# Optimization experiments

Measured on AMD Instinct MI355X. Metric: run time of the kernel, lower is better.

## Reference

```python
import jax, jax.numpy as jnp
import numpy as np

RADIUS = 0.4
NSHELLS = 3
GSCALE = 0.69314718056 * NSHELLS ** 2  # ln(2)*num_shells^2, as in TFN.__init__
KNN = 32          # patch_size
UNITS = 64        # per-type intertwiner width
STRIDE = 4        # source->target pooling ratio (num_points[i]/num_points[i+1])


def real_sh(d):
    """Real spherical harmonics up to l=3 on unit vectors d[...,3] -> [...,16]."""
    x, y, z = d[..., 0], d[..., 1], d[..., 2]
    x2, y2, z2 = x * x, y * y, z * z
    comps = [
        0.282095 * jnp.ones_like(x),                 # l=0
        0.488603 * y, 0.488603 * z, 0.488603 * x,    # l=1 (y,z,x)
        1.092548 * x * y,                            # l=2
        1.092548 * y * z,
        0.315392 * (3.0 * z2 - 1.0),
        1.092548 * x * z,
        0.546274 * (x2 - y2),
        0.590044 * y * (3.0 * x2 - y2),              # l=3
        2.890611 * x * y * z,
        0.457046 * y * (5.0 * z2 - 1.0),
        0.373176 * z * (5.0 * z2 - 3.0),
        0.457046 * x * (5.0 * z2 - 1.0),
        1.445306 * z * (x2 - y2),
        0.590044 * x * (x2 - 3.0 * y2),
    ]
    return jnp.stack(comps, axis=-1)


def setup_inputs() -> dict:
    key = jax.random.key(0)
    ks = jax.random.split(key, 16)
    B, N, C = 32, 2048, 64
    SC = NSHELLS * C  # channels after shell expansion
    FEAT = 4 * UNITS  # invariant feature dim (types 0..3)
    NUM_CLASSES = 40
    inp = {
        "points": jax.random.normal(ks[0], (B, N, 3), jnp.float32),
        "feats": 0.1 * jax.random.normal(ks[1], (B, N, C), jnp.float32),
        "W0": jax.random.normal(ks[2], (SC, UNITS), jnp.float32) / np.sqrt(SC),
        "b0": jnp.zeros((UNITS,), jnp.float32),
        "W1": jax.random.normal(ks[3], (SC, UNITS), jnp.float32) / np.sqrt(SC),
        "W2": jax.random.normal(ks[4], (SC, UNITS), jnp.float32) / np.sqrt(SC),
        "W3": jax.random.normal(ks[5], (SC, UNITS), jnp.float32) / np.sqrt(SC),
        "Wfc1": jax.random.normal(ks[6], (FEAT, 512), jnp.float32) / np.sqrt(FEAT),
        "bfc1": jnp.zeros((512,), jnp.float32),
        "Wfc2": jax.random.normal(ks[7], (512, 256), jnp.float32) / np.sqrt(512),
        "bfc2": jnp.zeros((256,), jnp.float32),
        "Wsm": jax.random.normal(ks[8], (256, NUM_CLASSES), jnp.float32) / np.sqrt(256),
        "bsm": jnp.zeros((NUM_CLASSES,), jnp.float32),
    }
    return inp


def reference(points, feats, W0, b0, W1, W2, W3, Wfc1, bfc1, Wfc2, bfc2, Wsm, bsm):
    # --- pooling: strided subsample (kd_pooling analogue) ---
    target = points[:, ::STRIDE]                       # [B,M,3]
    # --- ball-query style grouping: knn gather ---
    d2 = jnp.sum((target[:, :, None, :] - points[:, None, :, :]) ** 2, axis=-1)  # [B,M,N]
    _, idx = jax.lax.top_k(-d2, KNN)                   # [B,M,K]
    gat = jax.vmap(lambda a, i: a[i])
    p = gat(points, idx)                               # [B,M,K,3]
    f = gat(feats, idx)                                # [B,M,K,C]
    rel = p - target[:, :, None, :]
    dist = jnp.sqrt(jnp.maximum(jnp.sum(rel * rel, axis=-1), 1e-12))  # [B,M,K]
    dirs = rel / dist[..., None]
    # --- spherical-harmonic Gaussian shell kernels ---
    Y = real_sh(dirs)                                  # [B,M,K,16]
    centers = jnp.linspace(0.0, 1.0, NSHELLS)
    dn = dist / RADIUS
    w = jnp.exp(-GSCALE * (dn[..., None] - centers) ** 2)
    w = w * (dn <= 1.0)[..., None]                     # bounded kernel
    w = w / (jnp.sum(w, axis=2, keepdims=True) + 1e-8)  # normalize over patch
    kern = w[..., :, None] * Y[..., None, :]           # [B,M,K,S,16]
    # --- point conv: contract over patch dim ---
    z = jnp.einsum('bmksp,bmkc->bmpsc', kern, f)       # [B,M,16,S,C]
    B_, M_ = z.shape[:2]
    z = z.reshape(B_, M_, 16, -1)                      # [B,M,16,S*C]
    # --- per-type Dense intertwiners (bias only on type-0) + invariant norms ---
    slabs = [(0, 1, W0, b0), (1, 4, W1, None), (4, 9, W2, None), (9, 16, W3, None)]
    outs = []
    for s, e, W, b in slabs:
        o = z[:, :, s:e, :] @ W
        if b is not None:
            o = o + b
        outs.append(jnp.sqrt(jnp.maximum(jnp.sum(o * o, axis=2), 1e-8)))  # [B,M,U]
    h = jnp.concatenate(outs, axis=-1)                 # [B,M,4U]
    h = jnp.max(h, axis=1)                             # global max pool
    # --- MLP head ---
    h = jax.nn.relu(h @ Wfc1 + bfc1)
    h = jax.nn.relu(h @ Wfc2 + bfc2)
    return jax.nn.softmax(h @ Wsm + bsm, axis=-1)
```

## Files before the change

### kernel.cpp

```cpp
#include <hip/hip_runtime.h>
#include <hip/hip_bf16.h>
#include <math.h>

#define B_ 32
#define N_ 2048
#define C_ 64
#define M_ 512
#define KNN_ 32
#define RADIUS_ 0.4f
#define RCUT2 0.16016f
#define GSCALE_ 6.2383246250f
#define TT 4
#define NWAVE 8
#define SEGCAP 40
#define NBLK 4096

typedef __attribute__((ext_vector_type(8))) short bf16x8;
typedef __attribute__((ext_vector_type(4))) float f32x4;
union FragU { uint4 q; bf16x8 h; unsigned int u[4]; };

#define ZT_ 3208
#define ZTH (ZT_*2)
#define RSTH 200
#define ZLOFF 3200
#define FSH 560
#define CAND_OFF 6416
#define WGT_OFF  12832
#define WGT_TS   96
#define SM_TOTAL 13216

__device__ inline unsigned cvt_pk_bf16(float a, float b) {
    unsigned r;
    asm("v_cvt_pk_bf16_f32 %0, %1, %2" : "=v"(r) : "v"(a), "v"(b));
    return r;
}

__device__ inline void split_pair(float a0, float a1, unsigned& hw, unsigned& lw) {
    hw = cvt_pk_bf16(a0, a1);
    float r0 = a0 - __uint_as_float(hw << 16);
    float r1 = a1 - __uint_as_float(hw & 0xffff0000u);
    lw = cvt_pk_bf16(r0, r1);
}

__global__ __launch_bounds__(256) void wsplit_kernel(
    const float* __restrict__ W0, const float* __restrict__ W1,
    const float* __restrict__ W2, const float* __restrict__ W3,
    uint4* __restrict__ Wb)
{
    int gid = blockIdx.x * 256 + threadIdx.x;
    int lane = gid & 63, frag = gid >> 6;
    int nt = frag & 3;
    int ls = frag >> 2, ks = ls % 6, l = ls / 6;
    const float* W = (l==0) ? W0 : (l==1) ? W1 : (l==2) ? W2 : W3;
    int n = nt*16 + (lane & 15), quad = lane >> 4;
    unsigned int d[4];
    #pragma unroll
    for (int dd = 0; dd < 4; ++dd) {
        unsigned int two[2];
        #pragma unroll
        for (int e = 0; e < 2; ++e) {
            int k = ks*32 + quad*8 + dd*2 + e;
            __hip_bfloat16 hb = __float2bfloat16(W[k*64 + n]);
            two[e] = *(unsigned short*)&hb;
        }
        d[dd] = two[0] | (two[1] << 16);
    }
    Wb[(size_t)frag*64 + lane] = make_uint4(d[0], d[1], d[2], d[3]);
}

__global__ __launch_bounds__(512, 6) void main_kernel(
    const float* __restrict__ points, const float* __restrict__ feats,
    const float* __restrict__ b0, const uint4* __restrict__ Wb,
    unsigned int* __restrict__ hmax,
    const float* __restrict__ Wfc1, const float* __restrict__ Wfc2,
    float* __restrict__ dummy)
{
    __shared__ __align__(16) float smem[SM_TOTAL];
    __shared__ int sh_nbr[TT][32];
    __shared__ int sh_cnt[TT];
    __shared__ int cntk[NWAVE*TT];
    unsigned int* smemU = (unsigned int*)smem;
    unsigned short* smemH = (unsigned short*)smem;
    const int tid = threadIdx.x;
    const int b = blockIdx.x >> 7;
    const int mbase = (blockIdx.x & 127) * TT;
    const float* pb = points + (size_t)b * N_ * 3;
    const int wv = tid >> 6, lane = tid & 63;

    float wm1 = Wfc1[(size_t)blockIdx.x*32 + (tid & 31)];
    float wm2 = Wfc2[(size_t)blockIdx.x*32 + (tid & 31)];

    const int nh_pre = wv >> 2;
    float b0r[2];
    #pragma unroll
    for (int ntl = 0; ntl < 2; ++ntl)
        b0r[ntl] = b0[(nh_pre*2 + ntl)*16 + (lane & 15)];

    {
        unsigned long long* cand = (unsigned long long*)&smem[CAND_OFF];
        float tx[TT], ty[TT], tz[TT];
        #pragma unroll
        for (int c = 0; c < TT; ++c) {
            int m4 = 4*(mbase + c);
            tx[c] = pb[3*m4]; ty[c] = pb[3*m4+1]; tz[c] = pb[3*m4+2];
        }
        float px[4], py[4], pz[4];
        const float* ps = pb + 3*(wv*256 + lane);
        #pragma unroll
        for (int it = 0; it < 4; ++it) {
            px[it] = ps[it*192+0]; py[it] = ps[it*192+1]; pz[it] = ps[it*192+2];
        }
        int bcnt[TT];
        #pragma unroll
        for (int c = 0; c < TT; ++c) bcnt[c] = 0;
        #pragma unroll
        for (int it = 0; it < 4; ++it) {
            int i = wv*256 + it*64 + lane;
            #pragma unroll
            for (int c = 0; c < TT; ++c) {
                float dx = px[it] - tx[c], dy = py[it] - ty[c], dz = pz[it] - tz[c];
                float d2 = fmaf(dx,dx, fmaf(dy,dy, dz*dz));
                bool isc = d2 <= RCUT2;
                unsigned long long mk = __ballot(isc);
                if (isc) {
                    int pos = bcnt[c] + __popcll(mk & ((1ull<<lane)-1ull));
                    if (pos < SEGCAP)
                        cand[(size_t)(wv*TT+c)*SEGCAP + pos] =
                            ((unsigned long long)__float_as_uint(d2) << 32) | (unsigned)i;
                }
                bcnt[c] += __popcll(mk);
            }
        }
        if (lane == 0) {
            #pragma unroll
            for (int c = 0; c < TT; ++c)
                cntk[wv*TT+c] = bcnt[c] < SEGCAP ? bcnt[c] : SEGCAP;
        }
    }
    __syncthreads();

    if (wv < TT) {
        unsigned long long* cand = (unsigned long long*)&smem[CAND_OFF];
        const int t = wv;
        int os[NWAVE+1];
        os[0] = 0;
        #pragma unroll
        for (int w = 0; w < NWAVE; ++w) os[w+1] = os[w] + cntk[w*TT+t];
        int C = os[NWAVE] < 128 ? os[NWAVE] : 128;
        auto fetch = [&](int pos) -> unsigned long long {
            if (pos >= C) return ~0ull;
            int ws = 0, base = 0;
            #pragma unroll
            for (int w = 1; w < NWAVE; ++w)
                if (pos >= os[w]) { ws = w; base = os[w]; }
            return cand[(size_t)(ws*TT+t)*SEGCAP + (pos - base)];
        };
        unsigned long long kv0 = fetch(lane), kv1 = fetch(64 + lane);
        const unsigned long long lmask = (1ull << lane) - 1ull;
        if (C <= KNN_) {
            if (lane < KNN_) sh_nbr[t][lane] = (lane < C) ? (int)(kv0 & 0xffffffffu) : 0;
            if (lane == 0) sh_cnt[t] = C;
        } else {
            unsigned d0 = (unsigned)(kv0 >> 32);
            unsigned d1 = (unsigned)(kv1 >> 32);
            unsigned thr = 0u;
            for (int bit = 29; bit >= 0; --bit) {
                unsigned mid = thr | (1u << bit);
                int cnt = __popcll(__ballot(d0 < mid)) + __popcll(__ballot(d1 < mid));
                if (cnt < KNN_) thr = mid;
            }
            bool le0 = d0 < thr, le1 = d1 < thr;
            int cntL = __popcll(__ballot(le0)) + __popcll(__ballot(le1));
            int E = KNN_ - cntL;
            unsigned long long me0 = __ballot(d0 == thr);
            unsigned long long me1 = __ballot(d1 == thr);
            int e0 = __popcll(me0);
            bool sel0 = le0 || ((d0 == thr) && (__popcll(me0 & lmask) < E));
            bool sel1 = le1 || ((d1 == thr) && (e0 + __popcll(me1 & lmask) < E));
            unsigned long long ms0 = __ballot(sel0);
            if (sel0) sh_nbr[t][__popcll(ms0 & lmask)] = (int)(kv0 & 0xffffffffu);
            int base0 = __popcll(ms0);
            unsigned long long ms1 = __ballot(sel1);
            if (sel1) sh_nbr[t][base0 + __popcll(ms1 & lmask)] = (int)(kv1 & 0xffffffffu);
            if (lane == 0) sh_cnt[t] = KNN_;
        }
    }
    __syncthreads();

    {
        const int t = wv & 3, kh = wv >> 2;
        const float* fb = feats + (size_t)b * N_ * C_;
        float fv0[8], fv1[8];
        #pragma unroll
        for (int j = 0; j < 8; ++j) {
            int k2 = kh*8 + j;
            fv0[j] = fb[(size_t)sh_nbr[t][2*k2]   * C_ + lane];
            fv1[j] = fb[(size_t)sh_nbr[t][2*k2+1] * C_ + lane];
        }
        if (wv < TT && lane < 32) {
            int k = lane;
            int n = sh_nbr[t][k];
            int m4 = 4*(mbase + t);
            float x = pb[3*n]   - pb[3*m4];
            float y = pb[3*n+1] - pb[3*m4+1];
            float z = pb[3*n+2] - pb[3*m4+2];
            float d2 = x*x + y*y + z*z;
            float dist = sqrtf(fmaxf(d2, 1e-12f));
            float inv = 1.0f / dist;
            float dx = x*inv, dy = y*inv, dz = z*inv;
            float x2 = dx*dx, y2 = dy*dy, z2 = dz*dz;
            float yv[16];
            yv[0]  = 0.282095f;
            yv[1]  = 0.488603f*dy;  yv[2] = 0.488603f*dz;  yv[3] = 0.488603f*dx;
            yv[4]  = 1.092548f*dx*dy;
            yv[5]  = 1.092548f*dy*dz;
            yv[6]  = 0.315392f*(3.0f*z2-1.0f);
            yv[7]  = 1.092548f*dx*dz;
            yv[8]  = 0.546274f*(x2-y2);
            yv[9]  = 0.590044f*dy*(3.0f*x2-y2);
            yv[10] = 2.890611f*dx*dy*dz;
            yv[11] = 0.457046f*dy*(5.0f*z2-1.0f);
            yv[12] = 0.373176f*dz*(5.0f*z2-3.0f);
            yv[13] = 0.457046f*dx*(5.0f*z2-1.0f);
            yv[14] = 1.445306f*dz*(x2-y2);
            yv[15] = 0.590044f*dx*(x2-3.0f*y2);
            float* Yp = &smem[t*ZT_ + k*17];
            #pragma unroll
            for (int p = 0; p < 16; ++p) Yp[p] = yv[p];
            float dn = dist * (1.0f/RADIUS_);
            bool ok = (k < sh_cnt[t]) && (dn <= 1.0f);
            float w0 = 0.f, w1 = 0.f, w2 = 0.f;
            if (ok) {
                float dd0 = dn, dd1 = dn - 0.5f, dd2 = dn - 1.0f;
                w0 = __expf(-GSCALE_*dd0*dd0);
                w1 = __expf(-GSCALE_*dd1*dd1);
                w2 = __expf(-GSCALE_*dd2*dd2);
            }
            float s0 = w0, s1 = w1, s2 = w2;
            #pragma unroll
            for (int off = 16; off >= 1; off >>= 1) {
                s0 += __shfl_xor(s0, off);
                s1 += __shfl_xor(s1, off);
                s2 += __shfl_xor(s2, off);
            }
            w0 /= (s0 + 1e-8f);
            w1 /= (s1 + 1e-8f);
            w2 /= (s2 + 1e-8f);
            smem[WGT_OFF + t*WGT_TS +      k] = w0;
            smem[WGT_OFF + t*WGT_TS + 32 + k] = w1;
            smem[WGT_OFF + t*WGT_TS + 64 + k] = w2;
        }
        #pragma unroll
        for (int j = 0; j < 8; ++j) {
            int k2 = kh*8 + j;
            smemU[t*ZT_ + FSH + k2*66 + lane] = cvt_pk_bf16(fv0[j], fv1[j]);
        }
    }
    __syncthreads();

    f32x4 zacc[3][2];
    {
        const int t = wv & 3, nh = wv >> 2;
        const int quad = lane >> 4, col = lane & 15;
        float yv8[8];
        #pragma unroll
        for (int d = 0; d < 8; ++d)
            yv8[d] = smem[t*ZT_ + (quad*8 + d)*17 + col];
        FragU ah[3], al[3];
        #pragma unroll
        for (int s = 0; s < 3; ++s) {
            #pragma unroll
            for (int i = 0; i < 4; ++i) {
                float we = smem[WGT_OFF + t*WGT_TS + s*32 + quad*8 + 2*i];
                float wo = smem[WGT_OFF + t*WGT_TS + s*32 + quad*8 + 2*i + 1];
                split_pair(yv8[2*i]*we, yv8[2*i+1]*wo, ah[s].u[i], al[s].u[i]);
            }
        }
        #pragma unroll
        for (int s = 0; s < 3; ++s)
            #pragma unroll
            for (int nl = 0; nl < 2; ++nl) zacc[s][nl] = (f32x4){0.f,0.f,0.f,0.f};
        #pragma unroll
        for (int nl = 0; nl < 2; ++nl) {
            int n = (nh*2 + nl)*16 + col;
            FragU bh;
            #pragma unroll
            for (int i = 0; i < 4; ++i) {
                int k2 = quad*4 + i;
                bh.u[i] = smemU[t*ZT_ + FSH + k2*66 + n];
            }
            #pragma unroll
            for (int s = 0; s < 3; ++s) {
                zacc[s][nl] = __builtin_amdgcn_mfma_f32_16x16x32_bf16(ah[s].h, bh.h, zacc[s][nl], 0, 0, 0);
                zacc[s][nl] = __builtin_amdgcn_mfma_f32_16x16x32_bf16(al[s].h, bh.h, zacc[s][nl], 0, 0, 0);
            }
        }
    }
    __syncthreads();

    {
        const int t = wv & 3, nh = wv >> 2;
        const int quad = lane >> 4, col = lane & 15;
        #pragma unroll
        for (int s = 0; s < 3; ++s) {
            #pragma unroll
            for (int nl = 0; nl < 2; ++nl) {
                #pragma unroll
                for (int r = 0; r < 4; ++r) {
                    int p = quad*4 + r;
                    int j = s*64 + (nh*2+nl)*16 + col;
                    float a = zacc[s][nl][r];
                    unsigned th = cvt_pk_bf16(a, a);
                    smemH[t*ZTH + p*RSTH + j] = (unsigned short)th;
                    float res = a - __uint_as_float(th << 16);
                    unsigned tl_ = cvt_pk_bf16(res, res);
                    smemH[t*ZTH + ZLOFF + p*RSTH + j] = (unsigned short)tl_;
                }
            }
        }
    }

    {
        const int bp0[4] = {0,1,4,9};
        const int bsz[4] = {1,3,5,7};
        const int band = wv & 3, nh = wv >> 2;
        FragU bcur[2], bnxt[2];
        #pragma unroll
        for (int ntl = 0; ntl < 2; ++ntl)
            bcur[ntl].q = Wb[(size_t)((band*6 + 0)*4 + nh*2 + ntl)*64 + lane];
        __syncthreads();

        const int sz = bsz[band], p0 = bp0[band];
        const int rows = 2*sz;
        const int quad = lane >> 4, col = lane & 15;
        int gc = col < rows-1 ? col : rows-1;
        int tl = gc >= sz ? 1 : 0;
        int pA = p0 + gc - tl*sz;
        const unsigned hbA = tl*ZTH + pA*RSTH;
        const unsigned hbB = hbA + 2*ZTH;
        f32x4 acc[2][2];
        #pragma unroll
        for (int ti = 0; ti < 2; ++ti)
            #pragma unroll
            for (int ntl = 0; ntl < 2; ++ntl) acc[ti][ntl] = (f32x4){0.f,0.f,0.f,0.f};

        #pragma unroll
        for (int ks = 0; ks < 6; ++ks) {
            if (ks < 5) {
                #pragma unroll
                for (int ntl = 0; ntl < 2; ++ntl)
                    bnxt[ntl].q = Wb[(size_t)((band*6 + ks+1)*4 + nh*2 + ntl)*64 + lane];
            }
            FragU ahA, alA, ahB, alB;
            ahA.q = *(const uint4*)&smemH[hbA + ks*32 + quad*8];
            alA.q = *(const uint4*)&smemH[hbA + ZLOFF + ks*32 + quad*8];
            ahB.q = *(const uint4*)&smemH[hbB + ks*32 + quad*8];
            alB.q = *(const uint4*)&smemH[hbB + ZLOFF + ks*32 + quad*8];
            #pragma unroll
            for (int ntl = 0; ntl < 2; ++ntl) {
                acc[0][ntl] = __builtin_amdgcn_mfma_f32_16x16x32_bf16(ahA.h, bcur[ntl].h, acc[0][ntl], 0, 0, 0);
                acc[0][ntl] = __builtin_amdgcn_mfma_f32_16x16x32_bf16(alA.h, bcur[ntl].h, acc[0][ntl], 0, 0, 0);
                acc[1][ntl] = __builtin_amdgcn_mfma_f32_16x16x32_bf16(ahB.h, bcur[ntl].h, acc[1][ntl], 0, 0, 0);
                acc[1][ntl] = __builtin_amdgcn_mfma_f32_16x16x32_bf16(alB.h, bcur[ntl].h, acc[1][ntl], 0, 0, 0);
            }
            #pragma unroll
            for (int ntl = 0; ntl < 2; ++ntl) bcur[ntl] = bnxt[ntl];
        }
        float sq[2][4];
        #pragma unroll
        for (int ntl = 0; ntl < 2; ++ntl)
            #pragma unroll
            for (int tg = 0; tg < 4; ++tg) sq[ntl][tg] = 0.f;
        #pragma unroll
        for (int r = 0; r < 4; ++r) {
            int row = quad*4 + r;
            bool valid = row < rows;
            int tl2 = row >= sz ? 1 : 0;
            #pragma unroll
            for (int ti = 0; ti < 2; ++ti) {
                #pragma unroll
                for (int ntl = 0; ntl < 2; ++ntl) {
                    float o = acc[ti][ntl][r];
                    if (band == 0) o += b0r[ntl];
                    if (valid) sq[ntl][ti*2 + tl2] += o*o;
                }
            }
        }
        #pragma unroll
        for (int ntl = 0; ntl < 2; ++ntl) {
            #pragma unroll
            for (int tg = 0; tg < 4; ++tg) {
                float v = sq[ntl][tg];
                v += __shfl_xor(v, 16);
                v += __shfl_xor(v, 32);
                sq[ntl][tg] = v;
            }
        }
        if (quad == 0) {
            #pragma unroll
            for (int ntl = 0; ntl < 2; ++ntl) {
                float m = fmaxf(fmaxf(sq[ntl][0], sq[ntl][1]),
                                fmaxf(sq[ntl][2], sq[ntl][3]));
                float h = sqrtf(fmaxf(m, 1e-8f));
                atomicMax(&hmax[b*256 + band*64 + (nh*2 + ntl)*16 + col],
                          __float_as_uint(h) ^ 0x80000000u);
            }
        }
    }

    if (__float_as_uint(wm1 + wm2) == 0xdeadbeefu) dummy[0] = wm1;
}

__global__ __launch_bounds__(256) void fc1_kernel(
    const unsigned int* __restrict__ hmaxk,
    const float* __restrict__ Wfc1, const float* __restrict__ bfc1,
    float* __restrict__ t1)
{
    __shared__ float h[256];
    __shared__ float red[4][80];
    const int b = blockIdx.x >> 3, uc = blockIdx.x & 7;
    const int tid = threadIdx.x;
    const int u = tid & 63, iq = tid >> 6;
    h[tid] = __uint_as_float(hmaxk[b*256 + tid] ^ 0x80000000u);
    __syncthreads();
    float acc = 0.f;
    const float* Wp = Wfc1 + uc*64 + u;
    #pragma unroll 8
    for (int i = iq*64; i < iq*64 + 64; ++i)
        acc = fmaf(h[i], Wp[(size_t)i*512], acc);
    red[iq][u] = acc;
    __syncthreads();
    if (iq == 0) {
        float s = red[0][u] + red[1][u] + red[2][u] + red[3][u] + bfc1[uc*64 + u];
        t1[b*512 + uc*64 + u] = fmaxf(s, 0.f);
    }
}

__global__ __launch_bounds__(256) void fc2_kernel(
    const float* __restrict__ t1,
    const float* __restrict__ Wfc2, const float* __restrict__ bfc2,
    float* __restrict__ t2)
{
    __shared__ float t1s[512];
    __shared__ float red[4][80];
    const int b = blockIdx.x >> 2, uc = blockIdx.x & 3;
    const int tid = threadIdx.x;
    const int u = tid & 63, isl = tid >> 6;
    t1s[tid]       = t1[b*512 + tid];
    t1s[256 + tid] = t1[b*512 + 256 + tid];
    __syncthreads();
    float acc = 0.f;
    const float* Wp = Wfc2 + uc*64 + u;
    #pragma unroll 8
    for (int i = isl*128; i < isl*128 + 128; ++i)
        acc = fmaf(t1s[i], Wp[(size_t)i*256], acc);
    red[isl][u] = acc;
    __syncthreads();
    if (isl == 0) {
        float s = red[0][u] + red[1][u] + red[2][u] + red[3][u] + bfc2[uc*64 + u];
        t2[b*256 + uc*64 + u] = fmaxf(s, 0.f);
    }
}

__global__ __launch_bounds__(256) void fc3_kernel(
    const float* __restrict__ t2,
    const float* __restrict__ Wsm, const float* __restrict__ bsm,
    float* __restrict__ out)
{
    __shared__ float t2s[256];
    __shared__ float red[4][80];
    const int b = blockIdx.x;
    const int tid = threadIdx.x;
    const int u = tid & 63, isl = tid >> 6;
    t2s[tid] = t2[b*256 + tid];
    __syncthreads();
    float acc = 0.f;
    if (u < 40) {
        #pragma unroll 8
        for (int i = isl*64; i < isl*64 + 64; ++i)
            acc = fmaf(t2s[i], Wsm[(size_t)i*40 + u], acc);
    }
    red[isl][u] = acc;
    __syncthreads();
    if (tid < 64) {
        float s = red[0][tid] + red[1][tid] + red[2][tid] + red[3][tid];
        float x = (tid < 40) ? (s + bsm[tid]) : -1e30f;
        float mx = x;
        #pragma unroll
        for (int off = 32; off >= 1; off >>= 1) mx = fmaxf(mx, __shfl_xor(mx, off));
        float e = (tid < 40) ? expf(x - mx) : 0.f;
        float ssum = e;
        #pragma unroll
        for (int off = 32; off >= 1; off >>= 1) ssum += __shfl_xor(ssum, off);
        if (tid < 40) out[b*40 + tid] = e / ssum;
    }
}

extern "C" void kernel_launch(void* const* d_in, const int* in_sizes, int n_in,
                              void* d_out, int out_size, void* d_ws, size_t ws_size,
                              hipStream_t stream)
{
    const float* points = (const float*)d_in[0];
    const float* feats  = (const float*)d_in[1];
    const float* W0   = (const float*)d_in[2];
    const float* b0   = (const float*)d_in[3];
    const float* W1   = (const float*)d_in[4];
    const float* W2   = (const float*)d_in[5];
    const float* W3   = (const float*)d_in[6];
    const float* Wfc1 = (const float*)d_in[7];
    const float* bfc1 = (const float*)d_in[8];
    const float* Wfc2 = (const float*)d_in[9];
    const float* bfc2 = (const float*)d_in[10];
    const float* Wsm  = (const float*)d_in[11];
    const float* bsm  = (const float*)d_in[12];
    float* out = (float*)d_out;

    char* ws = (char*)d_ws;
    unsigned int* hmax = (unsigned int*)ws;
    float* t1 = (float*)(ws + 32*1024);
    float* t2 = (float*)(ws + 96*1024);
    float* dummy = (float*)(ws + 120*1024);
    uint4* Wb = (uint4*)(ws + 128*1024);

    wsplit_kernel<<<24, 256, 0, stream>>>(W0, W1, W2, W3, Wb);
    main_kernel<<<NBLK, 512, 0, stream>>>(points, feats, b0, Wb, hmax,
                                          Wfc1, Wfc2, dummy);
    fc1_kernel<<<256, 256, 0, stream>>>(hmax, Wfc1, bfc1, t1);
    fc2_kernel<<<128, 256, 0, stream>>>(t1, Wfc2, bfc2, t2);
    fc3_kernel<<<32, 256, 0, stream>>>(t2, Wsm, bsm, out);
}
```

Baseline: 165.7 us.

## Double block to 16 waves and use LDS atomics for candidate collection

Launches the main kernel with 1024 threads so each wave handles half as many points, feature rows and output column tiles. Neighbor candidate gathering now uses per-target shared-memory atomic counters into a single 128-slot list, replacing per-wave segmented lists and the prefix-offset fetch. This aims to raise latency hiding and cut per-wave register pressure, at the cost of LDS atomic contention, nondeterministic candidate order, and a tighter register cap from the launch bounds.

```diff
diff --git a/kernel.cpp b/kernel.cpp
--- a/kernel.cpp
+++ b/kernel.cpp
@@ -11,8 +11,8 @@
 #define RCUT2 0.16016f
 #define GSCALE_ 6.2383246250f
 #define TT 4
-#define NWAVE 8
-#define SEGCAP 40
+#define NWAVE 16
+#define CANDCAP 128
 #define NBLK 4096
 
 typedef __attribute__((ext_vector_type(8))) short bf16x8;
@@ -68,7 +68,7 @@
     Wb[(size_t)frag*64 + lane] = make_uint4(d[0], d[1], d[2], d[3]);
 }
 
-__global__ __launch_bounds__(512, 6) void main_kernel(
+__global__ __launch_bounds__(1024, 8) void main_kernel(
     const float* __restrict__ points, const float* __restrict__ feats,
     const float* __restrict__ b0, const uint4* __restrict__ Wb,
     unsigned int* __restrict__ hmax,
@@ -78,7 +78,7 @@
     __shared__ __align__(16) float smem[SM_TOTAL];
     __shared__ int sh_nbr[TT][32];
     __shared__ int sh_cnt[TT];
-    __shared__ int cntk[NWAVE*TT];
+    __shared__ int cnt4[TT];
     unsigned int* smemU = (unsigned int*)smem;
     unsigned short* smemH = (unsigned short*)smem;
     const int tid = threadIdx.x;
@@ -90,11 +90,10 @@
     float wm1 = Wfc1[(size_t)blockIdx.x*32 + (tid & 31)];
     float wm2 = Wfc2[(size_t)blockIdx.x*32 + (tid & 31)];
 
-    const int nh_pre = wv >> 2;
-    float b0r[2];
-    #pragma unroll
-    for (int ntl = 0; ntl < 2; ++ntl)
-        b0r[ntl] = b0[(nh_pre*2 + ntl)*16 + (lane & 15)];
+    float b0r = b0[(wv >> 2)*16 + (lane & 15)];
+
+    if (tid < TT) cnt4[tid] = 0;
+    __syncthreads();
 
     {
         unsigned long long* cand = (unsigned long long*)&smem[CAND_OFF];
@@ -104,37 +103,22 @@
             int m4 = 4*(mbase + c);
             tx[c] = pb[3*m4]; ty[c] = pb[3*m4+1]; tz[c] = pb[3*m4+2];
         }
-        float px[4], py[4], pz[4];
-        const float* ps = pb + 3*(wv*256 + lane);
-        #pragma unroll
-        for (int it = 0; it < 4; ++it) {
-            px[it] = ps[it*192+0]; py[it] = ps[it*192+1]; pz[it] = ps[it*192+2];
-        }
-        int bcnt[TT];
-        #pragma unroll
-        for (int c = 0; c < TT; ++c) bcnt[c] = 0;
-        #pragma unroll
-        for (int it = 0; it < 4; ++it) {
-            int i = wv*256 + it*64 + lane;
+        const float* ps = pb + 3*(wv*128 + lane);
+        #pragma unroll
+        for (int it = 0; it < 2; ++it) {
+            float px = ps[it*192+0], py = ps[it*192+1], pz = ps[it*192+2];
+            int i = wv*128 + it*64 + lane;
             #pragma unroll
             for (int c = 0; c < TT; ++c) {
-                float dx = px[it] - tx[c], dy = py[it] - ty[c], dz = pz[it] - tz[c];
+                float dx = px - tx[c], dy = py - ty[c], dz = pz - tz[c];
                 float d2 = fmaf(dx,dx, fmaf(dy,dy, dz*dz));
-                bool isc = d2 <= RCUT2;
-                unsigned long long mk = __ballot(isc);
-                if (isc) {
-                    int pos = bcnt[c] + __popcll(mk & ((1ull<<lane)-1ull));
-                    if (pos < SEGCAP)
-                        cand[(size_t)(wv*TT+c)*SEGCAP + pos] =
+                if (d2 <= RCUT2) {
+                    int slot = atomicAdd(&cnt4[c], 1);
+                    if (slot < CANDCAP)
+                        cand[(c<<7) + slot] =
                             ((unsigned long long)__float_as_uint(d2) << 32) | (unsigned)i;
                 }
-                bcnt[c] += __popcll(mk);
-            }
-        }
-        if (lane == 0) {
-            #pragma unroll
-            for (int c = 0; c < TT; ++c)
-                cntk[wv*TT+c] = bcnt[c] < SEGCAP ? bcnt[c] : SEGCAP;
+            }
         }
     }
     __syncthreads();
@@ -142,20 +126,9 @@
     if (wv < TT) {
         unsigned long long* cand = (unsigned long long*)&smem[CAND_OFF];
         const int t = wv;
-        int os[NWAVE+1];
-        os[0] = 0;
-        #pragma unroll
-        for (int w = 0; w < NWAVE; ++w) os[w+1] = os[w] + cntk[w*TT+t];
-        int C = os[NWAVE] < 128 ? os[NWAVE] : 128;
-        auto fetch = [&](int pos) -> unsigned long long {
-            if (pos >= C) return ~0ull;
-            int ws = 0, base = 0;
-            #pragma unroll
-            for (int w = 1; w < NWAVE; ++w)
-                if (pos >= os[w]) { ws = w; base = os[w]; }
-            return cand[(size_t)(ws*TT+t)*SEGCAP + (pos - base)];
-        };
-        unsigned long long kv0 = fetch(lane), kv1 = fetch(64 + lane);
+        int C = cnt4[t]; C = C < CANDCAP ? C : CANDCAP;
+        unsigned long long kv0 = (lane < C)      ? cand[(t<<7) + lane]      : ~0ull;
+        unsigned long long kv1 = (64 + lane < C) ? cand[(t<<7) + 64 + lane] : ~0ull;
         const unsigned long long lmask = (1ull << lane) - 1ull;
         if (C <= KNN_) {
             if (lane < KNN_) sh_nbr[t][lane] = (lane < C) ? (int)(kv0 & 0xffffffffu) : 0;
@@ -190,10 +163,10 @@
     {
         const int t = wv & 3, kh = wv >> 2;
         const float* fb = feats + (size_t)b * N_ * C_;
-        float fv0[8], fv1[8];
-        #pragma unroll
-        for (int j = 0; j < 8; ++j) {
-            int k2 = kh*8 + j;
+        float fv0[4], fv1[4];
+        #pragma unroll
+        for (int j = 0; j < 4; ++j) {
+            int k2 = kh*4 + j;
             fv0[j] = fb[(size_t)sh_nbr[t][2*k2]   * C_ + lane];
             fv1[j] = fb[(size_t)sh_nbr[t][2*k2+1] * C_ + lane];
         }
@@ -251,14 +224,14 @@
             smem[WGT_OFF + t*WGT_TS + 64 + k] = w2;
         }
         #pragma unroll
-        for (int j = 0; j < 8; ++j) {
-            int k2 = kh*8 + j;
+        for (int j = 0; j < 4; ++j) {
+            int k2 = kh*4 + j;
             smemU[t*ZT_ + FSH + k2*66 + lane] = cvt_pk_bf16(fv0[j], fv1[j]);
         }
     }
     __syncthreads();
 
-    f32x4 zacc[3][2];
+    f32x4 zacc[3];
     {
         const int t = wv & 3, nh = wv >> 2;
         const int quad = lane >> 4, col = lane & 15;
@@ -277,23 +250,18 @@
             }
         }
         #pragma unroll
-        for (int s = 0; s < 3; ++s)
-            #pragma unroll
-            for (int nl = 0; nl < 2; ++nl) zacc[s][nl] = (f32x4){0.f,0.f,0.f,0.f};
-        #pragma unroll
-        for (int nl = 0; nl < 2; ++nl) {
-            int n = (nh*2 + nl)*16 + col;
-            FragU bh;
-            #pragma unroll
-            for (int i = 0; i < 4; ++i) {
-                int k2 = quad*4 + i;
-                bh.u[i] = smemU[t*ZT_ + FSH + k2*66 + n];
-            }
-            #pragma unroll
-            for (int s = 0; s < 3; ++s) {
-                zacc[s][nl] = __builtin_amdgcn_mfma_f32_16x16x32_bf16(ah[s].h, bh.h, zacc[s][nl], 0, 0, 0);
-                zacc[s][nl] = __builtin_amdgcn_mfma_f32_16x16x32_bf16(al[s].h, bh.h, zacc[s][nl], 0, 0, 0);
-            }
+        for (int s = 0; s < 3; ++s) zacc[s] = (f32x4){0.f,0.f,0.f,0.f};
+        int n = nh*16 + col;
+        FragU bh;
+        #pragma unroll
+        for (int i = 0; i < 4; ++i) {
+            int k2 = quad*4 + i;
+            bh.u[i] = smemU[t*ZT_ + FSH + k2*66 + n];
+        }
+        #pragma unroll
+        for (int s = 0; s < 3; ++s) {
+            zacc[s] = __builtin_amdgcn_mfma_f32_16x16x32_bf16(ah[s].h, bh.h, zacc[s], 0, 0, 0);
+            zacc[s] = __builtin_amdgcn_mfma_f32_16x16x32_bf16(al[s].h, bh.h, zacc[s], 0, 0, 0);
         }
     }
     __syncthreads();
@@ -304,18 +272,15 @@
         #pragma unroll
         for (int s = 0; s < 3; ++s) {
             #pragma unroll
-            for (int nl = 0; nl < 2; ++nl) {
-                #pragma unroll
-                for (int r = 0; r < 4; ++r) {
-                    int p = quad*4 + r;
-                    int j = s*64 + (nh*2+nl)*16 + col;
-                    float a = zacc[s][nl][r];
-                    unsigned th = cvt_pk_bf16(a, a);
-                    smemH[t*ZTH + p*RSTH + j] = (unsigned short)th;
-                    float res = a - __uint_as_float(th << 16);
-                    unsigned tl_ = cvt_pk_bf16(res, res);
-                    smemH[t*ZTH + ZLOFF + p*RSTH + j] = (unsigned short)tl_;
-                }
+            for (int r = 0; r < 4; ++r) {
+                int p = quad*4 + r;
+                int j = s*64 + nh*16 + col;
+                float a = zacc[s][r];
+                unsigned th = cvt_pk_bf16(a, a);
+                smemH[t*ZTH + p*RSTH + j] = (unsigned short)th;
+                float res = a - __uint_as_float(th << 16);
+                unsigned tl_ = cvt_pk_bf16(res, res);
+                smemH[t*ZTH + ZLOFF + p*RSTH + j] = (unsigned short)tl_;
             }
         }
     }
@@ -323,11 +288,9 @@
     {
         const int bp0[4] = {0,1,4,9};
         const int bsz[4] = {1,3,5,7};
-        const int band = wv & 3, nh = wv >> 2;
-        FragU bcur[2], bnxt[2];
-        #pragma unroll
-        for (int ntl = 0; ntl < 2; ++ntl)
-            bcur[ntl].q = Wb[(size_t)((band*6 + 0)*4 + nh*2 + ntl)*64 + lane];
+        const int band = wv & 3, nq = wv >> 2;
+        FragU bcur, bnxt;
+        bcur.q = Wb[(size_t)((band*6 + 0)*4 + nq)*64 + lane];
         __syncthreads();
 
         const int sz = bsz[band], p0 = bp0[band];
@@ -338,39 +301,28 @@
         int pA = p0 + gc - tl*sz;
         const unsigned hbA = tl*ZTH + pA*RSTH;
         const unsigned hbB = hbA + 2*ZTH;
-        f32x4 acc[2][2];
-        #pragma unroll
-        for (int ti = 0; ti < 2; ++ti)
-            #pragma unroll
-            for (int ntl = 0; ntl < 2; ++ntl) acc[ti][ntl] = (f32x4){0.f,0.f,0.f,0.f};
+        f32x4 acc[2];
+        acc[0] = (f32x4){0.f,0.f,0.f,0.f};
+        acc[1] = (f32x4){0.f,0.f,0.f,0.f};
 
         #pragma unroll
         for (int ks = 0; ks < 6; ++ks) {
-            if (ks < 5) {
-                #pragma unroll
-                for (int ntl = 0; ntl < 2; ++ntl)
-                    bnxt[ntl].q = Wb[(size_t)((band*6 + ks+1)*4 + nh*2 + ntl)*64 + lane];
-            }
+            if (ks < 5)
+                bnxt.q = Wb[(size_t)((band*6 + ks+1)*4 + nq)*64 + lane];
             FragU ahA, alA, ahB, alB;
             ahA.q = *(const uint4*)&smemH[hbA + ks*32 + quad*8];
             alA.q = *(const uint4*)&smemH[hbA + ZLOFF + ks*32 + quad*8];
             ahB.q = *(const uint4*)&smemH[hbB + ks*32 + quad*8];
             alB.q = *(const uint4*)&smemH[hbB + ZLOFF + ks*32 + quad*8];
-            #pragma unroll
-            for (int ntl = 0; ntl < 2; ++ntl) {
-                acc[0][ntl] = __builtin_amdgcn_mfma_f32_16x16x32_bf16(ahA.h, bcur[ntl].h, acc[0][ntl], 0, 0, 0);
-                acc[0][ntl] = __builtin_amdgcn_mfma_f32_16x16x32_bf16(alA.h, bcur[ntl].h, acc[0][ntl], 0, 0, 0);
-                acc[1][ntl] = __builtin_amdgcn_mfma_f32_16x16x32_bf16(ahB.h, bcur[ntl].h, acc[1][ntl], 0, 0, 0);
-                acc[1][ntl] = __builtin_amdgcn_mfma_f32_16x16x32_bf16(alB.h, bcur[ntl].h, acc[1][ntl], 0, 0, 0);
-            }
-            #pragma unroll
-            for (int ntl = 0; ntl < 2; ++ntl) bcur[ntl] = bnxt[ntl];
-        }
-        float sq[2][4];
-        #pragma unroll
-        for (int ntl = 0; ntl < 2; ++ntl)
-            #pragma unroll
-            for (int tg = 0; tg < 4; ++tg) sq[ntl][tg] = 0.f;
+            acc[0] = __builtin_amdgcn_mfma_f32_16x16x32_bf16(ahA.h, bcur.h, acc[0], 0, 0, 0);
+            acc[0] = __builtin_amdgcn_mfma_f32_16x16x32_bf16(alA.h, bcur.h, acc[0], 0, 0, 0);
+            acc[1] = __builtin_amdgcn_mfma_f32_16x16x32_bf16(ahB.h, bcur.h, acc[1], 0, 0, 0);
+            acc[1] = __builtin_amdgcn_mfma_f32_16x16x32_bf16(alB.h, bcur.h, acc[1], 0, 0, 0);
+            bcur = bnxt;
+        }
+        float sq[4];
+        #pragma unroll
+        for (int tg = 0; tg < 4; ++tg) sq[tg] = 0.f;
         #pragma unroll
         for (int r = 0; r < 4; ++r) {
             int row = quad*4 + r;
@@ -378,33 +330,23 @@
             int tl2 = row >= sz ? 1 : 0;
             #pragma unroll
             for (int ti = 0; ti < 2; ++ti) {
-                #pragma unroll
-                for (int ntl = 0; ntl < 2; ++ntl) {
-                    float o = acc[ti][ntl][r];
-                    if (band == 0) o += b0r[ntl];
-                    if (valid) sq[ntl][ti*2 + tl2] += o*o;
-                }
-            }
-        }
-        #pragma unroll
-        for (int ntl = 0; ntl < 2; ++ntl) {
-            #pragma unroll
-            for (int tg = 0; tg < 4; ++tg) {
-                float v = sq[ntl][tg];
-                v += __shfl_xor(v, 16);
-                v += __shfl_xor(v, 32);
-                sq[ntl][tg] = v;
-            }
+                float o = acc[ti][r];
+                if (band == 0) o += b0r;
+                if (valid) sq[ti*2 + tl2] += o*o;
+            }
+        }
+        #pragma unroll
+        for (int tg = 0; tg < 4; ++tg) {
+            float v = sq[tg];
+            v += __shfl_xor(v, 16);
+            v += __shfl_xor(v, 32);
+            sq[tg] = v;
         }
         if (quad == 0) {
-            #pragma unroll
-            for (int ntl = 0; ntl < 2; ++ntl) {
-                float m = fmaxf(fmaxf(sq[ntl][0], sq[ntl][1]),
-                                fmaxf(sq[ntl][2], sq[ntl][3]));
-                float h = sqrtf(fmaxf(m, 1e-8f));
-                atomicMax(&hmax[b*256 + band*64 + (nh*2 + ntl)*16 + col],
-                          __float_as_uint(h) ^ 0x80000000u);
-            }
+            float m = fmaxf(fmaxf(sq[0], sq[1]), fmaxf(sq[2], sq[3]));
+            float h = sqrtf(fmaxf(m, 1e-8f));
+            atomicMax(&hmax[b*256 + band*64 + nq*16 + col],
+                      __float_as_uint(h) ^ 0x80000000u);
         }
     }
 
@@ -523,8 +465,8 @@
     uint4* Wb = (uint4*)(ws + 128*1024);
 
     wsplit_kernel<<<24, 256, 0, stream>>>(W0, W1, W2, W3, Wb);
-    main_kernel<<<NBLK, 512, 0, stream>>>(points, feats, b0, Wb, hmax,
-                                          Wfc1, Wfc2, dummy);
+    main_kernel<<<NBLK, 1024, 0, stream>>>(points, feats, b0, Wb, hmax,
+                                           Wfc1, Wfc2, dummy);
     fc1_kernel<<<256, 256, 0, stream>>>(hmax, Wfc1, bfc1, t1);
     fc2_kernel<<<128, 256, 0, stream>>>(t1, Wfc2, bfc2, t2);
     fc3_kernel<<<32, 256, 0, stream>>>(t2, Wsm, bsm, out);
```

Result: slower. 191.3 us (+15.5%).
